# Optimization experiments

Hardware: AMD Instinct MI355X
Metric: run time of the kernel (lower is better)

## Reference

```python
import jax, jax.numpy as jnp
import numpy as np

VOCAB = 400001  # vocab_size + 1
H = 100         # n_hidden
B = 512
T = 25
FC = 128
NC = 2
FORGET_BIAS = 1.0


def setup_inputs() -> dict:
    key = jax.random.key(0)
    ks = jax.random.split(key, 8)
    features = jax.random.randint(ks[0], (B, T), 0, VOCAB, dtype=jnp.int32)
    embedding = jax.random.normal(ks[1], (VOCAB, H), dtype=jnp.float32) * 0.05
    # BasicLSTMCell kernel: [input_dim + hidden, 4*hidden], gate order (i, j, f, o)
    k1 = jax.random.normal(ks[2], (2 * H, 4 * H), dtype=jnp.float32) * 0.05
    b1 = jnp.zeros((4 * H,), dtype=jnp.float32)
    k2 = jax.random.normal(ks[3], (2 * H, 4 * H), dtype=jnp.float32) * 0.05
    b2 = jnp.zeros((4 * H,), dtype=jnp.float32)
    w_fc1 = jax.random.normal(ks[4], (H, FC), dtype=jnp.float32) * 0.05
    b_fc1 = jnp.zeros((FC,), dtype=jnp.float32)
    w_fc2 = jax.random.normal(ks[5], (FC, NC), dtype=jnp.float32) * 0.05
    b_fc2 = jnp.zeros((NC,), dtype=jnp.float32)
    return {"features": features, "embedding": embedding,
            "k1": k1, "b1": b1, "k2": k2, "b2": b2,
            "w_fc1": w_fc1, "b_fc1": b_fc1, "w_fc2": w_fc2, "b_fc2": b_fc2}


def _lstm_cell(c, h, x, kernel, bias):
    z = jnp.concatenate([x, h], axis=-1) @ kernel + bias  # [B, 4H]
    i, j, f, o = jnp.split(z, 4, axis=-1)
    c_new = c * jax.nn.sigmoid(f + FORGET_BIAS) + jax.nn.sigmoid(i) * jnp.tanh(j)
    h_new = jnp.tanh(c_new) * jax.nn.sigmoid(o)
    return c_new, h_new


def reference(features, embedding, k1, b1, k2, b2, w_fc1, b_fc1, w_fc2, b_fc2):
    x = embedding[features]                      # [B, T, H]
    xs = jnp.swapaxes(x, 0, 1)                   # [T, B, H] for scan over time
    batch = features.shape[0]
    zeros = jnp.zeros((batch, H), dtype=embedding.dtype)

    def step(carry, xt):
        c1, h1, c2, h2 = carry
        c1, h1 = _lstm_cell(c1, h1, xt, k1, b1)
        c2, h2 = _lstm_cell(c2, h2, h1, k2, b2)
        return (c1, h1, c2, h2), None

    (c1, h1, c2, h2), _ = jax.lax.scan(step, (zeros, zeros, zeros, zeros), xs)
    # dynamic_rnn outputs[:, -1, :] == final top-layer hidden state h2
    fc1 = h2 @ w_fc1 + b_fc1                     # linear, no activation (tf.layers.dense default)
    pred = fc1 @ w_fc2 + b_fc2                   # [B, num_classes] logits
    return pred
```

## Files before the change

### kernel.cpp

```cpp
#include <hip/hip_runtime.h>
#include <cstdint>
#include <cstddef>

#define VOCABSZ 400001
#define Hn 100
#define Tn 25
#define Bn 512
#define FCn 128
#define Rr 2
#define NBLK (Bn / Rr)
#define NTHR 1024
#define RKQ 16

typedef _Float16 half2_t __attribute__((ext_vector_type(2)));

__device__ __forceinline__ half2_t h2bits(unsigned v) {
    union { unsigned u; half2_t h; } x; x.u = v; return x.h;
}
__device__ __forceinline__ float fdot2f(half2_t a, half2_t b, float c) {
    return __builtin_amdgcn_fdot2(a, b, c, false);
}
__device__ __forceinline__ float sigm(float x) {
    return __fdividef(1.0f, 1.0f + __expf(-x));
}
__device__ __forceinline__ float tanh_fast(float x) {
    float e = __expf(2.0f * x);
    return __fdividef(e - 1.0f, e + 1.0f);
}

__global__ void prep_weights(const float* __restrict__ k1,
                             const float* __restrict__ k2,
                             uint4* __restrict__ WP) {
    int t = blockIdx.x * blockDim.x + threadIdx.x;
    if (t >= 2 * 25 * 400) return;
    int l   = t / 10000;
    int rem = t % 10000;
    int kq  = rem / 400;
    int o   = rem % 400;
    int u = o >> 2, g = o & 3;
    int c = g * 100 + u;
    const float* K = l ? k2 : k1;
    union { unsigned u32; half2_t h; } d[4];
    #pragma unroll
    for (int j = 0; j < 4; j++) {
        int k0 = 8 * kq + 2 * j;
        d[j].h.x = (_Float16)K[(k0    ) * 400 + c];
        d[j].h.y = (_Float16)K[(k0 + 1) * 400 + c];
    }
    uint4 v; v.x = d[0].u32; v.y = d[1].u32; v.z = d[2].u32; v.w = d[3].u32;
    WP[t] = v;
}

__device__ __forceinline__ float lstm_update(float z, int g, float& cst) {
    float t1 = __shfl_xor(z, 1);
    float t2 = __shfl_xor(z, 2);
    float t3 = __shfl_xor(t1, 2);
    bool g0 = (g & 1) != 0, g1 = (g & 2) != 0;
    float vi = g1 ? (g0 ? t3 : t2) : (g0 ? t1 : z);
    float vj = g1 ? (g0 ? t2 : t3) : (g0 ? z  : t1);
    float vf = g1 ? (g0 ? t1 : z ) : (g0 ? t3 : t2);
    float vo = g1 ? (g0 ? z  : t1) : (g0 ? t2 : t3);
    cst = cst * sigm(vf + 1.0f) + sigm(vi) * tanh_fast(vj);
    return tanh_fast(cst) * sigm(vo);
}

__device__ __forceinline__ void gemv2(const _Float16* s0,
                                      const _Float16* s1,
                                      const uint4* wreg,
                                      const uint4* __restrict__ wp,
                                      float bias, float& Z0, float& Z1) {
    const uint4* p0 = (const uint4*)s0;
    const uint4* p1 = (const uint4*)s1;
    float a0 = 0.f, a1 = 0.f, a2 = 0.f, a3 = 0.f;
    float d0 = 0.f, d1 = 0.f, d2 = 0.f, d3 = 0.f;
    #pragma unroll
    for (int kq = RKQ; kq < 25; kq++) {
        uint4 wv = wp[kq * 400];
        uint4 vx = p0[kq];
        uint4 vy = p1[kq];
        a0 = fdot2f(h2bits(wv.x), h2bits(vx.x), a0);
        a1 = fdot2f(h2bits(wv.y), h2bits(vx.y), a1);
        a2 = fdot2f(h2bits(wv.z), h2bits(vx.z), a2);
        a3 = fdot2f(h2bits(wv.w), h2bits(vx.w), a3);
        d0 = fdot2f(h2bits(wv.x), h2bits(vy.x), d0);
        d1 = fdot2f(h2bits(wv.y), h2bits(vy.y), d1);
        d2 = fdot2f(h2bits(wv.z), h2bits(vy.z), d2);
        d3 = fdot2f(h2bits(wv.w), h2bits(vy.w), d3);
    }
    #pragma unroll
    for (int kq = 0; kq < RKQ; kq++) {
        uint4 wv = wreg[kq];
        uint4 vx = p0[kq];
        uint4 vy = p1[kq];
        a0 = fdot2f(h2bits(wv.x), h2bits(vx.x), a0);
        a1 = fdot2f(h2bits(wv.y), h2bits(vx.y), a1);
        a2 = fdot2f(h2bits(wv.z), h2bits(vx.z), a2);
        a3 = fdot2f(h2bits(wv.w), h2bits(vx.w), a3);
        d0 = fdot2f(h2bits(wv.x), h2bits(vy.x), d0);
        d1 = fdot2f(h2bits(wv.y), h2bits(vy.y), d1);
        d2 = fdot2f(h2bits(wv.z), h2bits(vy.z), d2);
        d3 = fdot2f(h2bits(wv.w), h2bits(vy.w), d3);
    }
    Z0 = (a0 + a1) + (a2 + a3) + bias;
    Z1 = (d0 + d1) + (d2 + d3) + bias;
}

__global__ __launch_bounds__(NTHR, 1) void lstm_main(
    const int*   __restrict__ features,
    const float* __restrict__ embedding,
    const float* __restrict__ b1,
    const float* __restrict__ b2,
    const float* __restrict__ w_fc1,
    const float* __restrict__ b_fc1,
    const float* __restrict__ w_fc2,
    const float* __restrict__ b_fc2,
    const uint4* __restrict__ WP,
    float*       __restrict__ out)
{
    __shared__ __align__(16) _Float16 xh1[2][Rr][200];
    __shared__ __align__(16) _Float16 xh2[2][Rr][200];
    __shared__ float wred[8][2];

    const int tid  = threadIdx.x;
    const int lane = tid & 63;
    const int l    = tid >> 9;
    const int ht   = tid & 511;
    const int o    = (ht < 400) ? ht : 399;
    const int u = o >> 2, g = o & 3;
    const int c = g * 100 + u;
    const bool owner  = (ht < 400);
    const bool active = (ht < 448);

    const uint4* wp = WP + (size_t)(l * 25) * 400 + o;
    uint4 wreg[RKQ];
    #pragma unroll
    for (int kq = 0; kq < RKQ; kq++)
        wreg[kq] = wp[kq * 400];

    const float bias = (l ? b2 : b1)[c];

    if (tid < 200) {
        int r = tid / 100, uu = tid % 100;
        xh1[0][r][100 + uu] = (_Float16)0.0f;
        xh2[1][r][100 + uu] = (_Float16)0.0f;
    }
    if (tid < 100) {
        int r = tid / 50, p = tid % 50;
        int f0 = features[(blockIdx.x * Rr + r) * Tn + 0];
        float2 e = *(const float2*)(embedding + (size_t)f0 * Hn + 2 * p);
        half2_t h; h.x = (_Float16)e.x; h.y = (_Float16)e.y;
        ((half2_t*)&xh1[0][r][0])[p] = h;
    }
    __syncthreads();

    float cst[Rr] = {0.f, 0.f};
    float hv[Rr]  = {0.f, 0.f};

    for (int ph = 0; ph <= Tn; ph++) {
        const int p  = ph & 1;
        const int wb = p ^ 1;
        const bool dorun = active && (l ? (ph >= 1) : (ph < Tn));
        if (dorun) {
            float2 epre = {0.f, 0.f};
            int prow = 0, pp = 0;
            if (l == 0 && owner && g == 1 && ph + 1 < Tn) {
                prow = (u >= 50);
                pp   = u % 50;
                int f1 = features[(blockIdx.x * Rr + prow) * Tn + ph + 1];
                epre = *(const float2*)(embedding + (size_t)f1 * Hn + 2 * pp);
            }
            const _Float16* s0 = l ? &xh2[p][0][0] : &xh1[p][0][0];
            const _Float16* s1 = l ? &xh2[p][1][0] : &xh1[p][1][0];
            float z0, z1;
            gemv2(s0, s1, wreg, wp, bias, z0, z1);
            hv[0] = lstm_update(z0, g, cst[0]);
            hv[1] = lstm_update(z1, g, cst[1]);
            if (l == 0 && owner) {
                if (g == 0) {
                    xh1[wb][0][100 + u] = (_Float16)hv[0];
                    xh1[wb][1][100 + u] = (_Float16)hv[1];
                    xh2[wb][0][u]       = (_Float16)hv[0];
                    xh2[wb][1][u]       = (_Float16)hv[1];
                }
                if (g == 1 && ph + 1 < Tn) {
                    half2_t h; h.x = (_Float16)epre.x; h.y = (_Float16)epre.y;
                    ((half2_t*)&xh1[wb][prow][0])[pp] = h;
                }
            }
            if (l == 1 && owner && g == 0) {
                xh2[wb][0][100 + u] = (_Float16)hv[0];
                xh2[wb][1][100 + u] = (_Float16)hv[1];
            }
        }
        __syncthreads();
    }

    if (tid < Rr * FCn) {
        int r = tid >> 7;
        int j = tid & 127;
        float acc = b_fc1[j];
        #pragma unroll 10
        for (int uu = 0; uu < Hn; uu++)
            acc = fmaf((float)xh2[0][r][100 + uu], w_fc1[uu * FCn + j], acc);
        float p0 = acc * w_fc2[2 * j + 0];
        float p1 = acc * w_fc2[2 * j + 1];
        #pragma unroll
        for (int off = 32; off > 0; off >>= 1) {
            p0 += __shfl_down(p0, off, 64);
            p1 += __shfl_down(p1, off, 64);
        }
        if (lane == 0) {
            int wv = tid >> 6;
            wred[wv][0] = p0;
            wred[wv][1] = p1;
        }
    }
    __syncthreads();
    if (tid < 4) {
        int r = tid >> 1, cls = tid & 1;
        out[(blockIdx.x * Rr + r) * 2 + cls] =
            wred[2 * r][cls] + wred[2 * r + 1][cls] + b_fc2[cls];
    }
}

extern "C" void kernel_launch(void* const* d_in, const int* in_sizes, int n_in,
                              void* d_out, int out_size, void* d_ws, size_t ws_size,
                              hipStream_t stream) {
    const int*   features  = (const int*)  d_in[0];
    const float* embedding = (const float*)d_in[1];
    const float* k1        = (const float*)d_in[2];
    const float* b1        = (const float*)d_in[3];
    const float* k2        = (const float*)d_in[4];
    const float* b2        = (const float*)d_in[5];
    const float* w_fc1     = (const float*)d_in[6];
    const float* b_fc1     = (const float*)d_in[7];
    const float* w_fc2     = (const float*)d_in[8];
    const float* b_fc2     = (const float*)d_in[9];

    uint4* WP = (uint4*)d_ws;

    prep_weights<<<(20000 + 255) / 256, 256, 0, stream>>>(k1, k2, WP);
    lstm_main<<<NBLK, NTHR, 0, stream>>>(features, embedding, b1, b2,
                                         w_fc1, b_fc1, w_fc2, b_fc2,
                                         WP, (float*)d_out);
}
```

Baseline: 329.5 us.

## Stage LSTM weight chunks in LDS and cut register-resident weights

Lowers the number of weight chunks held in registers per thread from 16 to 6. Layer 1's remaining 19 chunks and 4 of layer 2's are copied into shared memory once at kernel start. Layer 2 reads its last 15 chunks from global memory (L2) on every step. The aim is to relieve register pressure and take most per-step global weight loads off the recurrent critical path. The cost is about 147KB of LDS per block, an uneven split of work between the two layers, and more global traffic for layer 2.

```diff
diff --git a/kernel.cpp b/kernel.cpp
--- a/kernel.cpp
+++ b/kernel.cpp
@@ -10,7 +10,11 @@
 #define Rr 2
 #define NBLK (Bn / Rr)
 #define NTHR 1024
-#define RKQ 16
+
+#define RKQ   6
+#define L1LDS 19
+#define L2LDS 4
+#define WLCH  (L1LDS + L2LDS)
 
 typedef _Float16 half2_t __attribute__((ext_vector_type(2)));
 
@@ -64,20 +68,33 @@
     return tanh_fast(cst) * sigm(vo);
 }
 
-__device__ __forceinline__ void gemv2(const _Float16* s0,
-                                      const _Float16* s1,
-                                      const uint4* wreg,
-                                      const uint4* __restrict__ wp,
-                                      float bias, float& Z0, float& Z1) {
-    const uint4* p0 = (const uint4*)s0;
-    const uint4* p1 = (const uint4*)s1;
+template<int NG>
+__device__ __forceinline__ void gemv(const uint4* p0, const uint4* p1,
+                                     const uint4* wreg, const uint4* lw,
+                                     const uint4* __restrict__ gw,
+                                     float bias, float& Z0, float& Z1) {
+    constexpr int NLDS = 19 - NG;
     float a0 = 0.f, a1 = 0.f, a2 = 0.f, a3 = 0.f;
     float d0 = 0.f, d1 = 0.f, d2 = 0.f, d3 = 0.f;
     #pragma unroll
-    for (int kq = RKQ; kq < 25; kq++) {
-        uint4 wv = wp[kq * 400];
-        uint4 vx = p0[kq];
-        uint4 vy = p1[kq];
+    for (int t = 0; t < NG; t++) {
+        uint4 wv = gw[t * 400];
+        uint4 vx = p0[RKQ + NLDS + t];
+        uint4 vy = p1[RKQ + NLDS + t];
+        a0 = fdot2f(h2bits(wv.x), h2bits(vx.x), a0);
+        a1 = fdot2f(h2bits(wv.y), h2bits(vx.y), a1);
+        a2 = fdot2f(h2bits(wv.z), h2bits(vx.z), a2);
+        a3 = fdot2f(h2bits(wv.w), h2bits(vx.w), a3);
+        d0 = fdot2f(h2bits(wv.x), h2bits(vy.x), d0);
+        d1 = fdot2f(h2bits(wv.y), h2bits(vy.y), d1);
+        d2 = fdot2f(h2bits(wv.z), h2bits(vy.z), d2);
+        d3 = fdot2f(h2bits(wv.w), h2bits(vy.w), d3);
+    }
+    #pragma unroll
+    for (int t = 0; t < NLDS; t++) {
+        uint4 wv = lw[t * 400];
+        uint4 vx = p0[RKQ + t];
+        uint4 vy = p1[RKQ + t];
         a0 = fdot2f(h2bits(wv.x), h2bits(vx.x), a0);
         a1 = fdot2f(h2bits(wv.y), h2bits(vx.y), a1);
         a2 = fdot2f(h2bits(wv.z), h2bits(vx.z), a2);
@@ -117,6 +134,7 @@
     const uint4* __restrict__ WP,
     float*       __restrict__ out)
 {
+    __shared__ __align__(16) uint4    WL[WLCH * 400];
     __shared__ __align__(16) _Float16 xh1[2][Rr][200];
     __shared__ __align__(16) _Float16 xh2[2][Rr][200];
     __shared__ float wred[8][2];
@@ -137,7 +155,18 @@
     for (int kq = 0; kq < RKQ; kq++)
         wreg[kq] = wp[kq * 400];
 
+    const uint4* lw = &WL[(l ? L1LDS * 400 : 0) + o];
+    const uint4* gw = wp + (RKQ + L2LDS) * 400;
+
     const float bias = (l ? b2 : b1)[c];
+
+    for (int idx = tid; idx < WLCH * 400; idx += NTHR) {
+        int i  = idx / 400;
+        int oo = idx - i * 400;
+        int ll = (i < L1LDS) ? 0 : 1;
+        int kk = (i < L1LDS) ? (RKQ + i) : (RKQ + i - L1LDS);
+        WL[idx] = WP[(ll * 25 + kk) * 400 + oo];
+    }
 
     if (tid < 200) {
         int r = tid / 100, uu = tid % 100;
@@ -169,10 +198,11 @@
                 int f1 = features[(blockIdx.x * Rr + prow) * Tn + ph + 1];
                 epre = *(const float2*)(embedding + (size_t)f1 * Hn + 2 * pp);
             }
-            const _Float16* s0 = l ? &xh2[p][0][0] : &xh1[p][0][0];
-            const _Float16* s1 = l ? &xh2[p][1][0] : &xh1[p][1][0];
+            const uint4* p0 = (const uint4*)(l ? &xh2[p][0][0] : &xh1[p][0][0]);
+            const uint4* p1 = (const uint4*)(l ? &xh2[p][1][0] : &xh1[p][1][0]);
             float z0, z1;
-            gemv2(s0, s1, wreg, wp, bias, z0, z1);
+            if (l == 0) gemv<0> (p0, p1, wreg, lw, gw, bias, z0, z1);
+            else        gemv<15>(p0, p1, wreg, lw, gw, bias, z0, z1);
             hv[0] = lstm_update(z0, g, cst[0]);
             hv[1] = lstm_update(z1, g, cst[1]);
             if (l == 0 && owner) {
```

New measurement: 325.8 us. Within noise of the previous version (-1.1%).
